# Kernel tuning notes

Measured on AMD Instinct MI355X. Metric: run time of the kernel, lower is better.

The kernel has to match this reference:

```python
import jax, jax.numpy as jnp
import numpy as np

B, T, C, H = 4, 2048, 1024, 16


def setup_inputs() -> dict:
    key = jax.random.key(0)
    ks = jax.random.split(key, 5)
    s_attn = 1.0 / np.sqrt(C)
    s_proj = 1.0 / np.sqrt(C)
    return {
        "x": jax.random.normal(ks[0], (B, T, C), dtype=jnp.float32),
        "w_attn": jax.random.uniform(ks[1], (3 * C, C), dtype=jnp.float32, minval=-s_attn, maxval=s_attn),
        "b_attn": jax.random.uniform(ks[2], (3 * C,), dtype=jnp.float32, minval=-s_attn, maxval=s_attn),
        "w_proj": jax.random.uniform(ks[3], (C, C), dtype=jnp.float32, minval=-s_proj, maxval=s_proj),
        "b_proj": jax.random.uniform(ks[4], (C,), dtype=jnp.float32, minval=-s_proj, maxval=s_proj),
    }


def reference(x, w_attn, b_attn, w_proj, b_proj):
    b, t, c = x.shape
    hd = c // H  # head dim
    qkv = jnp.einsum('btc,dc->btd', x, w_attn) + b_attn  # [B,T,3C]
    q, k, v = jnp.split(qkv, 3, axis=-1)
    # [B,H,T,hd]
    q = q.reshape(b, t, H, hd).transpose(0, 2, 1, 3)
    k = k.reshape(b, t, H, hd).transpose(0, 2, 1, 3)
    v = v.reshape(b, t, H, hd).transpose(0, 2, 1, 3)
    att = jnp.einsum('bhqd,bhkd->bhqk', q, k) * (1.0 / np.sqrt(hd))
    mask = jnp.tril(jnp.ones((t, t), dtype=bool))  # causal
    att = jnp.where(mask, att, -jnp.inf)
    att = jax.nn.softmax(att, axis=-1)
    y = jnp.einsum('bhqk,bhkd->bhqd', att, v)
    y = y.transpose(0, 2, 1, 3).reshape(b, t, c)
    return jnp.einsum('btc,dc->btd', y, w_proj) + b_proj
```

## Files before the change

### kernel.cpp

```cpp
#include <hip/hip_runtime.h>

#define Bb 4
#define Tt 2048
#define Cc 1024
#define Hh 16
#define NQKV 3072
#define Mtot 8192

typedef __bf16 bf16_t;
typedef unsigned short u16;
typedef __bf16 bf16x8 __attribute__((ext_vector_type(8)));
typedef __bf16 bf16x4 __attribute__((ext_vector_type(4)));
typedef short short4v __attribute__((ext_vector_type(4)));
typedef float f32x4 __attribute__((ext_vector_type(4)));
typedef float f32x16 __attribute__((ext_vector_type(16)));
typedef unsigned uint2v __attribute__((ext_vector_type(2)));

union bfu { bf16_t b; u16 u; };
union trpair { short4v h[2]; bf16x8 v; };
union pfu { unsigned u[4]; bf16x8 v; };

#define QSCALE 0.18033688011112042f

#define TRD(dst, addr, OFF)                                                     \
  asm volatile("ds_read_b64_tr_b16 %0, %1 offset:" OFF                          \
               : "=v"(dst) : "v"(addr) : "memory")

__device__ __forceinline__ unsigned cvtpk(float a, float b) {
  unsigned r;
  asm("v_cvt_pk_bf16_f32 %0, %1, %2" : "=v"(r) : "v"(a), "v"(b));
  return r;
}
__device__ __forceinline__ uint2v plswap(unsigned a, unsigned b) {
  return __builtin_amdgcn_permlane32_swap(a, b, false, false);
}

__global__ __launch_bounds__(256) void cvt_f32_bf16(const float* __restrict__ s,
                                                    u16* __restrict__ d,
                                                    long nscale, float factor) {
  size_t i = ((size_t)blockIdx.x * 256 + threadIdx.x) * 8;
  const float f = ((long)i < nscale) ? factor : 1.0f;
  float4 a = *(const float4*)(s + i);
  float4 b = *(const float4*)(s + i + 4);
  bf16x8 v;
  v[0]=(bf16_t)(a.x*f); v[1]=(bf16_t)(a.y*f); v[2]=(bf16_t)(a.z*f); v[3]=(bf16_t)(a.w*f);
  v[4]=(bf16_t)(b.x*f); v[5]=(bf16_t)(b.y*f); v[6]=(bf16_t)(b.z*f); v[7]=(bf16_t)(b.w*f);
  *(bf16x8*)(d + i) = v;
}

__global__ __launch_bounds__(256) void scale_bias(const float* __restrict__ s,
                                                  float* __restrict__ d) {
  int i = blockIdx.x * 256 + threadIdx.x;
  d[i] = s[i] * ((i < Cc) ? QSCALE : 1.0f);
}

template <int OUTBF16>
__global__ __launch_bounds__(256) void gemm_bf16(
    const u16* __restrict__ A, const u16* __restrict__ Bm,
    const float* __restrict__ bias, void* __restrict__ Cout,
    int M, int N, int K)
{
  __shared__ __attribute__((aligned(16))) u16 sa[128][40];
  __shared__ __attribute__((aligned(16))) u16 sb[128][40];

  const int tid  = threadIdx.x;
  const int lane = tid & 63;
  const int wid  = tid >> 6;
  const int wr   = (wid >> 1) * 64;
  const int wc   = (wid & 1) * 64;
  const int l15  = lane & 15;
  const int lh   = lane >> 4;
  const int bm   = blockIdx.x * 128;
  const int bn   = blockIdx.y * 128;

  f32x4 acc[4][4] = {};

  const int srow = tid >> 1;
  const int sseg = (tid & 1) * 16;

  const u16* pa = A  + (size_t)(bm + srow) * K + sseg;
  const u16* pb = Bm + (size_t)(bn + srow) * K + sseg;

  uint4 ar0 = *(const uint4*)pa, ar1 = *(const uint4*)(pa + 8);
  uint4 br0 = *(const uint4*)pb, br1 = *(const uint4*)(pb + 8);
  pa += 32; pb += 32;

  for (int k0 = 0; k0 < K; k0 += 32) {
    __syncthreads();
    *(uint4*)&sa[srow][sseg]     = ar0;
    *(uint4*)&sa[srow][sseg + 8] = ar1;
    *(uint4*)&sb[srow][sseg]     = br0;
    *(uint4*)&sb[srow][sseg + 8] = br1;
    __syncthreads();
    if (k0 + 32 < K) {
      ar0 = *(const uint4*)pa; ar1 = *(const uint4*)(pa + 8);
      br0 = *(const uint4*)pb; br1 = *(const uint4*)(pb + 8);
      pa += 32; pb += 32;
    }
    bf16x8 af[4], bfv[4];
#pragma unroll
    for (int mi = 0; mi < 4; mi++)
      af[mi] = *(const bf16x8*)&sa[wr + mi*16 + l15][lh * 8];
#pragma unroll
    for (int ni = 0; ni < 4; ni++)
      bfv[ni] = *(const bf16x8*)&sb[wc + ni*16 + l15][lh * 8];
#pragma unroll
    for (int mi = 0; mi < 4; mi++)
#pragma unroll
      for (int ni = 0; ni < 4; ni++)
        acc[mi][ni] = __builtin_amdgcn_mfma_f32_16x16x32_bf16(
            af[mi], bfv[ni], acc[mi][ni], 0, 0, 0);
  }

#pragma unroll
  for (int mi = 0; mi < 4; mi++) {
#pragma unroll
    for (int ni = 0; ni < 4; ni++) {
      const int col = bn + wc + ni*16 + l15;
      const float bs = bias[col];
#pragma unroll
      for (int r = 0; r < 4; r++) {
        const int row = bm + wr + mi*16 + lh*4 + r;
        const float val = acc[mi][ni][r] + bs;
        if (OUTBF16) {
          bfu cv; cv.b = (bf16_t)val;
          ((u16*)Cout)[(size_t)row * N + col] = cv.u;
        } else {
          ((float*)Cout)[(size_t)row * N + col] = val;
        }
      }
    }
  }
}

#define V0u 4608
__global__ __launch_bounds__(256) void attn_kernel(
    const u16* __restrict__ qkv, u16* __restrict__ y)
{
  __shared__ __attribute__((aligned(16))) u16 smem[9216];

  const int tid  = threadIdx.x;
  const int lane = tid & 63;
  const int w    = tid >> 6;
  const int l31  = lane & 31;
  const int hh   = lane >> 5;
  const int l15  = lane & 15;
  const int lh   = lane >> 4;
  const int bh   = blockIdx.y;
  const int b    = bh >> 4;
  const int head = bh & 15;

  const size_t rowbase = (size_t)b * Tt * NQKV;

  const int skey = tid >> 2;
  const int sp   = tid & 3;
  const u16* kbase = qkv + rowbase + 1024 + head*64 + sp*16;
  const u16* vbase = qkv + rowbase + 2048 + head*64 + sp*16;

  const unsigned smemB = (unsigned)(size_t)(&smem[0]);
  const unsigned vaddr = smemB + 2*V0u
      + ((lh>>1)*8 + (l15>>2))*144 + (lh&1)*32 + (l15&3)*8;

  for (int half = 0; half < 2; ++half) {
    const int qb    = half ? (15 - (int)blockIdx.x) : (int)blockIdx.x;
    const int qbase = qb * 128;
    const int qw    = qbase + w * 32;
    const int qi    = qw + l31;
    const int ktiles = 2*qb + 2;

    bf16x8 qfrag[4];
#pragma unroll
    for (int m = 0; m < 4; ++m)
      qfrag[m] = *(const bf16x8*)(qkv + rowbase + (size_t)qi * NQKV
                                  + head*64 + m*16 + hh*8);

    f32x16 o0 = {}, o1 = {};
    float m_run = -1e30f, l_part = 0.0f;

    uint4 kr0 = *(const uint4*)(kbase + (size_t)skey * NQKV);
    uint4 kr1 = *(const uint4*)(kbase + (size_t)skey * NQKV + 8);
    uint4 vr0 = *(const uint4*)(vbase + (size_t)skey * NQKV);
    uint4 vr1 = *(const uint4*)(vbase + (size_t)skey * NQKV + 8);

    for (int kt = 0; kt < ktiles; ++kt) {
      __syncthreads();
      *(uint4*)&smem[skey*72 + sp*16]           = kr0;
      *(uint4*)&smem[skey*72 + sp*16 + 8]       = kr1;
      *(uint4*)&smem[V0u + skey*72 + sp*16]     = vr0;
      *(uint4*)&smem[V0u + skey*72 + sp*16 + 8] = vr1;
      __syncthreads();

      if (kt + 1 < ktiles) {
        const u16* kp = kbase + (size_t)((kt+1)*64 + skey) * NQKV;
        const u16* vp = vbase + (size_t)((kt+1)*64 + skey) * NQKV;
        kr0 = *(const uint4*)kp; kr1 = *(const uint4*)(kp + 8);
        vr0 = *(const uint4*)vp; vr1 = *(const uint4*)(vp + 8);
      }

      if (kt*64 <= qw + 31) {
        f32x16 s0 = {}, s1 = {};
#pragma unroll
        for (int m = 0; m < 4; ++m) {
          bf16x8 k0 = *(const bf16x8*)&smem[(l31)*72      + m*16 + hh*8];
          bf16x8 k1 = *(const bf16x8*)&smem[(32 + l31)*72 + m*16 + hh*8];
          s0 = __builtin_amdgcn_mfma_f32_32x32x16_bf16(k0, qfrag[m], s0, 0,0,0);
          s1 = __builtin_amdgcn_mfma_f32_32x32x16_bf16(k1, qfrag[m], s1, 0,0,0);
        }

        if (kt*64 + 63 > qw) {
          const int kb0 = kt*64;
#pragma unroll
          for (int r = 0; r < 16; ++r) {
            const int crow = (r&3) + 8*(r>>2) + 4*hh;
            if (kb0 + crow > qi)      s0[r] = -1e30f;
            if (kb0 + 32 + crow > qi) s1[r] = -1e30f;
          }
        }

        float rm = s0[0];
#pragma unroll
        for (int r = 1; r < 16; ++r) rm = fmaxf(rm, s0[r]);
#pragma unroll
        for (int r = 0; r < 16; ++r) rm = fmaxf(rm, s1[r]);
        {
          uint2v t = plswap(__float_as_uint(rm), __float_as_uint(rm));
          rm = fmaxf(__uint_as_float(t[0]), __uint_as_float(t[1]));
        }
        if (__any(rm > m_run + 8.0f)) {
          const float mn = fmaxf(m_run, rm);
          const float al = exp2f(m_run - mn);
          m_run = mn; l_part *= al;
#pragma unroll
          for (int r = 0; r < 16; ++r) { o0[r] *= al; o1[r] *= al; }
        }

        pfu pf0, pf1, pf2, pf3;
        {
          float pe[16];
#pragma unroll
          for (int r = 0; r < 16; ++r) { pe[r] = exp2f(s0[r] - m_run); l_part += pe[r]; }
          unsigned a0 = cvtpk(pe[0],pe[1]),  a1 = cvtpk(pe[2],pe[3]);
          unsigned a2 = cvtpk(pe[4],pe[5]),  a3 = cvtpk(pe[6],pe[7]);
          uint2v x1 = plswap(a0, a2), x2 = plswap(a1, a3);
          pf0.u[0]=x1[0]; pf0.u[1]=x2[0]; pf0.u[2]=x1[1]; pf0.u[3]=x2[1];
          unsigned b0 = cvtpk(pe[8],pe[9]),  b1 = cvtpk(pe[10],pe[11]);
          unsigned b2 = cvtpk(pe[12],pe[13]), b3 = cvtpk(pe[14],pe[15]);
          uint2v x3 = plswap(b0, b2), x4 = plswap(b1, b3);
          pf1.u[0]=x3[0]; pf1.u[1]=x4[0]; pf1.u[2]=x3[1]; pf1.u[3]=x4[1];
        }
        {
          float pe[16];
#pragma unroll
          for (int r = 0; r < 16; ++r) { pe[r] = exp2f(s1[r] - m_run); l_part += pe[r]; }
          unsigned a0 = cvtpk(pe[0],pe[1]),  a1 = cvtpk(pe[2],pe[3]);
          unsigned a2 = cvtpk(pe[4],pe[5]),  a3 = cvtpk(pe[6],pe[7]);
          uint2v x1 = plswap(a0, a2), x2 = plswap(a1, a3);
          pf2.u[0]=x1[0]; pf2.u[1]=x2[0]; pf2.u[2]=x1[1]; pf2.u[3]=x2[1];
          unsigned b0 = cvtpk(pe[8],pe[9]),  b1 = cvtpk(pe[10],pe[11]);
          unsigned b2 = cvtpk(pe[12],pe[13]), b3 = cvtpk(pe[14],pe[15]);
          uint2v x3 = plswap(b0, b2), x4 = plswap(b1, b3);
          pf3.u[0]=x3[0]; pf3.u[1]=x4[0]; pf3.u[2]=x3[1]; pf3.u[3]=x4[1];
        }

        short4v ta0,tb0,ta1,tb1,ta2,tb2,ta3,tb3,ta4,tb4,ta5,tb5,ta6,tb6,ta7,tb7;
        TRD(ta0, vaddr, "0");    TRD(tb0, vaddr, "576");
        TRD(ta1, vaddr, "64");   TRD(tb1, vaddr, "640");
        TRD(ta2, vaddr, "2304"); TRD(tb2, vaddr, "2880");
        TRD(ta3, vaddr, "2368"); TRD(tb3, vaddr, "2944");
        TRD(ta4, vaddr, "4608"); TRD(tb4, vaddr, "5184");
        TRD(ta5, vaddr, "4672"); TRD(tb5, vaddr, "5248");
        TRD(ta6, vaddr, "6912"); TRD(tb6, vaddr, "7488");
        TRD(ta7, vaddr, "6976"); TRD(tb7, vaddr, "7552");
        asm volatile("s_waitcnt lgkmcnt(0)" ::: "memory");
        __builtin_amdgcn_sched_barrier(0);
        trpair v00,v01,v10,v11,v20,v21,v30,v31;
        v00.h[0]=ta0; v00.h[1]=tb0;  v01.h[0]=ta1; v01.h[1]=tb1;
        v10.h[0]=ta2; v10.h[1]=tb2;  v11.h[0]=ta3; v11.h[1]=tb3;
        v20.h[0]=ta4; v20.h[1]=tb4;  v21.h[0]=ta5; v21.h[1]=tb5;
        v30.h[0]=ta6; v30.h[1]=tb6;  v31.h[0]=ta7; v31.h[1]=tb7;
        o0 = __builtin_amdgcn_mfma_f32_32x32x16_bf16(v00.v, pf0.v, o0, 0,0,0);
        o1 = __builtin_amdgcn_mfma_f32_32x32x16_bf16(v01.v, pf0.v, o1, 0,0,0);
        o0 = __builtin_amdgcn_mfma_f32_32x32x16_bf16(v10.v, pf1.v, o0, 0,0,0);
        o1 = __builtin_amdgcn_mfma_f32_32x32x16_bf16(v11.v, pf1.v, o1, 0,0,0);
        o0 = __builtin_amdgcn_mfma_f32_32x32x16_bf16(v20.v, pf2.v, o0, 0,0,0);
        o1 = __builtin_amdgcn_mfma_f32_32x32x16_bf16(v21.v, pf2.v, o1, 0,0,0);
        o0 = __builtin_amdgcn_mfma_f32_32x32x16_bf16(v30.v, pf3.v, o0, 0,0,0);
        o1 = __builtin_amdgcn_mfma_f32_32x32x16_bf16(v31.v, pf3.v, o1, 0,0,0);
      }
    }

    {
      uint2v t = plswap(__float_as_uint(l_part), __float_as_uint(l_part));
      l_part = __uint_as_float(t[0]) + __uint_as_float(t[1]);
    }
    const float inv = 1.0f / l_part;

    __syncthreads();
#pragma unroll
    for (int k4 = 0; k4 < 4; ++k4) {
      bf16x4 pa, pb;
#pragma unroll
      for (int j = 0; j < 4; ++j) {
        pa[j] = (bf16_t)(o0[4*k4 + j] * inv);
        pb[j] = (bf16_t)(o1[4*k4 + j] * inv);
      }
      *(bf16x4*)&smem[w*2304 + l31*72 +      8*k4 + 4*hh] = pa;
      *(bf16x4*)&smem[w*2304 + l31*72 + 32 + 8*k4 + 4*hh] = pb;
    }
    u16* yp = y + ((size_t)(b*Tt + qi)) * Cc + head*64;
#pragma unroll
    for (int p = 0; p < 4; ++p) {
      bf16x8 row = *(const bf16x8*)&smem[w*2304 + l31*72 + p*16 + hh*8];
      *(bf16x8*)(yp + p*16 + hh*8) = row;
    }
  }
}

extern "C" void kernel_launch(void* const* d_in, const int* in_sizes, int n_in,
                              void* d_out, int out_size, void* d_ws, size_t ws_size,
                              hipStream_t stream) {
  const float* x      = (const float*)d_in[0];
  const float* w_attn = (const float*)d_in[1];
  const float* b_attn = (const float*)d_in[2];
  const float* w_proj = (const float*)d_in[3];
  const float* b_proj = (const float*)d_in[4];
  float* out = (float*)d_out;

  char* ws = (char*)d_ws;
  u16*   xb    = (u16*)(ws + 0);
  u16*   wab   = (u16*)(ws + 16777216);
  u16*   wpb   = (u16*)(ws + 23068672);
  u16*   qkvb  = (u16*)(ws + 25165824);
  u16*   yb    = (u16*)(ws + 75497472);
  float* sbias = (float*)(ws + 92274688);

  cvt_f32_bf16<<<4096, 256, 0, stream>>>(x,      xb,  0, 1.0f);
  cvt_f32_bf16<<<1536, 256, 0, stream>>>(w_attn, wab, (long)Cc*Cc, QSCALE);
  cvt_f32_bf16<<<512,  256, 0, stream>>>(w_proj, wpb, 0, 1.0f);
  scale_bias<<<12, 256, 0, stream>>>(b_attn, sbias);

  gemm_bf16<1><<<dim3(Mtot/128, NQKV/128), 256, 0, stream>>>(
      xb, wab, sbias, (void*)qkvb, Mtot, NQKV, Cc);

  attn_kernel<<<dim3(8, Bb*Hh), 256, 0, stream>>>(qkvb, yb);

  gemm_bf16<0><<<dim3(Mtot/128, Cc/128), 256, 0, stream>>>(
      yb, wpb, b_proj, (void*)out, Mtot, Cc, Cc);
}
```

Before: 192.3 us.

## Double attention query tile to 256 rows per block and fuse conversion kernels

The attention kernel now runs 512-thread blocks that each cover 256 queries instead of 128. Each K/V tile loaded into shared memory is reused by 8 waves instead of 4, and the grid shrinks to 256 blocks, keeping the pairing of a front and back chunk to balance causal work. The three fp32-to-bf16 conversions and the bias scaling are merged into one launch to cut launch overhead. The cost is a single block per CU with a larger shared allocation, which reduces the scheduler's ability to overlap work across blocks and leaves less slack for load imbalance.

```diff
diff --git a/kernel.cpp b/kernel.cpp
--- a/kernel.cpp
+++ b/kernel.cpp
@@ -35,11 +35,7 @@
   return __builtin_amdgcn_permlane32_swap(a, b, false, false);
 }
 
-__global__ __launch_bounds__(256) void cvt_f32_bf16(const float* __restrict__ s,
-                                                    u16* __restrict__ d,
-                                                    long nscale, float factor) {
-  size_t i = ((size_t)blockIdx.x * 256 + threadIdx.x) * 8;
-  const float f = ((long)i < nscale) ? factor : 1.0f;
+__device__ __forceinline__ void cvt8(const float* s, u16* d, size_t i, float f) {
   float4 a = *(const float4*)(s + i);
   float4 b = *(const float4*)(s + i + 4);
   bf16x8 v;
@@ -48,10 +44,30 @@
   *(bf16x8*)(d + i) = v;
 }
 
-__global__ __launch_bounds__(256) void scale_bias(const float* __restrict__ s,
-                                                  float* __restrict__ d) {
-  int i = blockIdx.x * 256 + threadIdx.x;
-  d[i] = s[i] * ((i < Cc) ? QSCALE : 1.0f);
+__global__ __launch_bounds__(256) void cvt_all(
+    const float* __restrict__ x, const float* __restrict__ w_attn,
+    const float* __restrict__ w_proj, const float* __restrict__ b_attn,
+    u16* __restrict__ xb, u16* __restrict__ wab, u16* __restrict__ wpb,
+    float* __restrict__ sbias)
+{
+  const int blk = blockIdx.x;
+  if (blk < 4096) {
+    size_t i = ((size_t)blk * 256 + threadIdx.x) * 8;
+    cvt8(x, xb, i, 1.0f);
+  } else if (blk < 5632) {
+    size_t i = ((size_t)(blk - 4096) * 256 + threadIdx.x) * 8;
+    cvt8(w_attn, wab, i, (i < (size_t)Cc * Cc) ? QSCALE : 1.0f);
+  } else if (blk < 6144) {
+    size_t i = ((size_t)(blk - 5632) * 256 + threadIdx.x) * 8;
+    cvt8(w_proj, wpb, i, 1.0f);
+  } else {
+    int i0 = (blk - 6144) * 2048 + threadIdx.x * 8;
+#pragma unroll
+    for (int j = 0; j < 8; ++j) {
+      int i = i0 + j;
+      if (i < NQKV) sbias[i] = b_attn[i] * ((i < Cc) ? QSCALE : 1.0f);
+    }
+  }
 }
 
 template <int OUTBF16>
@@ -133,11 +149,10 @@
   }
 }
 
-#define V0u 4608
-__global__ __launch_bounds__(256) void attn_kernel(
+__global__ __launch_bounds__(512, 4) void attn_kernel(
     const u16* __restrict__ qkv, u16* __restrict__ y)
 {
-  __shared__ __attribute__((aligned(16))) u16 smem[9216];
+  __shared__ __attribute__((aligned(16))) u16 smem[18432];
 
   const int tid  = threadIdx.x;
   const int lane = tid & 63;
@@ -152,21 +167,21 @@
 
   const size_t rowbase = (size_t)b * Tt * NQKV;
 
-  const int skey = tid >> 2;
-  const int sp   = tid & 3;
-  const u16* kbase = qkv + rowbase + 1024 + head*64 + sp*16;
-  const u16* vbase = qkv + rowbase + 2048 + head*64 + sp*16;
+  const int skey = tid >> 3;
+  const int sp   = tid & 7;
+  const u16* kbase = qkv + rowbase + 1024 + head*64 + sp*8;
+  const u16* vbase = qkv + rowbase + 2048 + head*64 + sp*8;
 
   const unsigned smemB = (unsigned)(size_t)(&smem[0]);
-  const unsigned vaddr = smemB + 2*V0u
+  const unsigned vaddr = smemB + 9216
       + ((lh>>1)*8 + (l15>>2))*144 + (lh&1)*32 + (l15&3)*8;
 
   for (int half = 0; half < 2; ++half) {
-    const int qb    = half ? (15 - (int)blockIdx.x) : (int)blockIdx.x;
-    const int qbase = qb * 128;
+    const int qx    = half ? (7 - (int)blockIdx.x) : (int)blockIdx.x;
+    const int qbase = qx * 256;
     const int qw    = qbase + w * 32;
     const int qi    = qw + l31;
-    const int ktiles = 2*qb + 2;
+    const int ktiles = 4*qx + 4;
 
     bf16x8 qfrag[4];
 #pragma unroll
@@ -178,31 +193,26 @@
     float m_run = -1e30f, l_part = 0.0f;
 
     uint4 kr0 = *(const uint4*)(kbase + (size_t)skey * NQKV);
-    uint4 kr1 = *(const uint4*)(kbase + (size_t)skey * NQKV + 8);
     uint4 vr0 = *(const uint4*)(vbase + (size_t)skey * NQKV);
-    uint4 vr1 = *(const uint4*)(vbase + (size_t)skey * NQKV + 8);
 
     for (int kt = 0; kt < ktiles; ++kt) {
       __syncthreads();
-      *(uint4*)&smem[skey*72 + sp*16]           = kr0;
-      *(uint4*)&smem[skey*72 + sp*16 + 8]       = kr1;
-      *(uint4*)&smem[V0u + skey*72 + sp*16]     = vr0;
-      *(uint4*)&smem[V0u + skey*72 + sp*16 + 8] = vr1;
+      *(uint4*)&smem[skey*72 + sp*8]        = kr0;
+      *(uint4*)&smem[4608 + skey*72 + sp*8] = vr0;
       __syncthreads();
 
       if (kt + 1 < ktiles) {
-        const u16* kp = kbase + (size_t)((kt+1)*64 + skey) * NQKV;
-        const u16* vp = vbase + (size_t)((kt+1)*64 + skey) * NQKV;
-        kr0 = *(const uint4*)kp; kr1 = *(const uint4*)(kp + 8);
-        vr0 = *(const uint4*)vp; vr1 = *(const uint4*)(vp + 8);
+        kr0 = *(const uint4*)(kbase + (size_t)((kt+1)*64 + skey) * NQKV);
+        vr0 = *(const uint4*)(vbase + (size_t)((kt+1)*64 + skey) * NQKV);
       }
 
       if (kt*64 <= qw + 31) {
         f32x16 s0 = {}, s1 = {};
 #pragma unroll
         for (int m = 0; m < 4; ++m) {
-          bf16x8 k0 = *(const bf16x8*)&smem[(l31)*72      + m*16 + hh*8];
-          bf16x8 k1 = *(const bf16x8*)&smem[(32 + l31)*72 + m*16 + hh*8];
+          const int co = m*16 + hh*8;
+          bf16x8 k0 = *(const bf16x8*)&smem[(l31)*72      + co];
+          bf16x8 k1 = *(const bf16x8*)&smem[(32 + l31)*72 + co];
           s0 = __builtin_amdgcn_mfma_f32_32x32x16_bf16(k0, qfrag[m], s0, 0,0,0);
           s1 = __builtin_amdgcn_mfma_f32_32x32x16_bf16(k1, qfrag[m], s1, 0,0,0);
         }
@@ -334,15 +344,13 @@
   u16*   yb    = (u16*)(ws + 75497472);
   float* sbias = (float*)(ws + 92274688);
 
-  cvt_f32_bf16<<<4096, 256, 0, stream>>>(x,      xb,  0, 1.0f);
-  cvt_f32_bf16<<<1536, 256, 0, stream>>>(w_attn, wab, (long)Cc*Cc, QSCALE);
-  cvt_f32_bf16<<<512,  256, 0, stream>>>(w_proj, wpb, 0, 1.0f);
-  scale_bias<<<12, 256, 0, stream>>>(b_attn, sbias);
+  cvt_all<<<6146, 256, 0, stream>>>(x, w_attn, w_proj, b_attn,
+                                    xb, wab, wpb, sbias);
 
   gemm_bf16<1><<<dim3(Mtot/128, NQKV/128), 256, 0, stream>>>(
       xb, wab, sbias, (void*)qkvb, Mtot, NQKV, Cc);
 
-  attn_kernel<<<dim3(8, Bb*Hh), 256, 0, stream>>>(qkvb, yb);
+  attn_kernel<<<dim3(4, Bb*Hh), 512, 0, stream>>>(qkvb, yb);
 
   gemm_bf16<0><<<dim3(Mtot/128, Cc/128), 256, 0, stream>>>(
       yb, wpb, b_proj, (void*)out, Mtot, Cc, Cc);
```

After: 184.8 us. -3.9%, faster.
